# Optimization experiments

Hardware: AMD Instinct MI355X
Metric: run time of the kernel (lower is better)

## Reference

```python
import jax, jax.numpy as jnp
import numpy as np

N = 8192
K = 8192
BS = 128  # quantization block size (elements per codebook)
NE = 8    # codebook entries per block (3-bit indices)


def setup_inputs() -> dict:
    key = jax.random.key(0)
    k1, k2, k3 = jax.random.split(key, 3)
    num_blocks = N * K // BS  # 524288
    n_packed_bytes = num_blocks * BS * 3 // 8  # 25165824
    x = jax.random.normal(k1, (2048, K), dtype=jnp.float32)
    # random packed bytes (values 0..255) -> uniformly random 3-bit indices
    packed_indices = jax.random.randint(k2, (n_packed_bytes,), 0, 256, dtype=jnp.int32)
    codebook = jax.random.normal(k3, (num_blocks, NE), dtype=jnp.float32)
    return {"x": x, "packed_indices": packed_indices, "codebook": codebook}


def _dequantize(packed_indices, codebook):
    num_blocks = codebook.shape[0]
    packed = packed_indices.reshape(-1, 3).astype(jnp.int32)  # (n_groups, 3)
    bits24 = packed[:, 0] | (packed[:, 1] << 8) | (packed[:, 2] << 16)
    shifts = jnp.arange(8, dtype=jnp.int32) * 3
    idx = (bits24[:, None] >> shifts[None, :]) & 7          # (n_groups, 8)
    idx = idx.reshape(num_blocks, BS)                        # (num_blocks, BS)
    # per-block codebook gather: w[b, i] = codebook[b, idx[b, i]]
    w = jnp.take_along_axis(codebook, idx, axis=1)           # (num_blocks, BS)
    return w.reshape(N, K)


def reference(x, packed_indices, codebook):
    w = _dequantize(packed_indices, codebook)  # (N, K) fp32
    y = x @ w.T                                # (batch, N)
    return y
```

## Files before the change

### kernel.cpp

```cpp
#include <hip/hip_runtime.h>
#include <hip/hip_bf16.h>

#define Mdim 2048
#define Ndim 8192
#define Kdim 8192
#define BM 128
#define BN 128
#define BK 64

typedef __bf16 bf16x8 __attribute__((ext_vector_type(8)));
typedef float f32x4 __attribute__((ext_vector_type(4)));
typedef unsigned short ushort8 __attribute__((ext_vector_type(8)));

__device__ __forceinline__ unsigned short f2bf_rne(float f) {
    unsigned u = __float_as_uint(f);
    u += 0x7fffu + ((u >> 16) & 1u);
    return (unsigned short)(u >> 16);
}

#define DQG 1024
__global__ __launch_bounds__(256) void k_dequant(const int* __restrict__ packed,
                                                 const float* __restrict__ cb,
                                                 unsigned short* __restrict__ W) {
    __shared__ int sp[3 * DQG];
    const int t = threadIdx.x;
    const size_t gbase = (size_t)blockIdx.x * DQG;
    const int4* pv = (const int4*)(packed + gbase * 3);
    int4* sv = (int4*)sp;
    sv[t]       = pv[t];
    sv[t + 256] = pv[t + 256];
    sv[t + 512] = pv[t + 512];
    __syncthreads();
#pragma unroll
    for (int c = 0; c < 4; ++c) {
        const int g = t + 256 * c;
        int p0 = sp[3 * g + 0];
        int p1 = sp[3 * g + 1];
        int p2 = sp[3 * g + 2];
        unsigned bits = (unsigned)(p0 & 255) | ((unsigned)(p1 & 255) << 8) |
                        ((unsigned)(p2 & 255) << 16);
        const size_t gg = gbase + g;
        const float4* cv = (const float4*)(cb + ((gg >> 4) << 3));
        float4 c0 = cv[0];
        float4 c1 = cv[1];
        ushort8 o;
#pragma unroll
        for (int i = 0; i < 8; ++i) {
            unsigned id = (bits >> (3 * i)) & 7u;
            float a0 = (id & 1) ? c0.y : c0.x;
            float a1 = (id & 1) ? c0.w : c0.z;
            float a2 = (id & 1) ? c1.y : c1.x;
            float a3 = (id & 1) ? c1.w : c1.z;
            float b0 = (id & 2) ? a1 : a0;
            float b1 = (id & 2) ? a3 : a2;
            float v  = (id & 4) ? b1 : b0;
            o[i] = f2bf_rne(v);
        }
        *(ushort8*)(W + (gg << 3)) = o;
    }
}

__global__ __launch_bounds__(256) void k_cvt(const float* __restrict__ x,
                                             unsigned short* __restrict__ xb) {
    size_t t = (size_t)blockIdx.x * 256 + threadIdx.x;
    const float4* xv = (const float4*)x;
    float4 a = xv[2 * t + 0];
    float4 b = xv[2 * t + 1];
    ushort8 o;
    o[0] = f2bf_rne(a.x); o[1] = f2bf_rne(a.y); o[2] = f2bf_rne(a.z); o[3] = f2bf_rne(a.w);
    o[4] = f2bf_rne(b.x); o[5] = f2bf_rne(b.y); o[6] = f2bf_rne(b.z); o[7] = f2bf_rne(b.w);
    ((ushort8*)xb)[t] = o;
}

__device__ __forceinline__ void gld16(const unsigned short* g, unsigned short* l) {
    __builtin_amdgcn_global_load_lds(
        (const __attribute__((address_space(1))) unsigned int*)g,
        (__attribute__((address_space(3))) unsigned int*)l, 16, 0, 0);
}

__global__ __launch_bounds__(256) void k_gemm(const unsigned short* __restrict__ A,
                                              const unsigned short* __restrict__ B,
                                              float* __restrict__ C) {
    __shared__ unsigned short As[BM * BK];
    __shared__ unsigned short Bs[BN * BK];

    const int tid  = threadIdx.x;
    const int lane = tid & 63;
    const int wave = tid >> 6;
    const int waveM = wave >> 1;
    const int waveN = wave & 1;
    const int bm = blockIdx.y * BM;
    const int bn = blockIdx.x * BN;

    const int srow = tid >> 3;
    const int scol = (((tid & 7) ^ ((tid >> 3) & 7))) * 8;
    const unsigned short* agp = A + (size_t)(bm + srow) * Kdim + scol;
    const unsigned short* bgp = B + (size_t)(bn + srow) * Kdim + scol;
    unsigned short* alp = &As[tid * 8];
    unsigned short* blp = &Bs[tid * 8];

    f32x4 acc[4][4];
    const f32x4 zero = {0.f, 0.f, 0.f, 0.f};
#pragma unroll
    for (int i = 0; i < 4; ++i)
#pragma unroll
        for (int j = 0; j < 4; ++j) acc[i][j] = zero;

    const int r15 = lane & 15;
    const int q   = lane >> 4;
    const int rlo = r15 & 7;

    for (int kt = 0; kt < Kdim; kt += BK) {
#pragma unroll
        for (int j = 0; j < 4; ++j) {
            gld16(agp + (size_t)(j * 32) * Kdim + kt, alp + j * 2048);
            gld16(bgp + (size_t)(j * 32) * Kdim + kt, blp + j * 2048);
        }
        __syncthreads();

#pragma unroll
        for (int kk = 0; kk < 2; ++kk) {
            const int slot = ((kk * 4 + q) ^ rlo) * 8;
            bf16x8 af[4], bfr[4];
#pragma unroll
            for (int i = 0; i < 4; ++i)
                af[i] = *(const bf16x8*)(&As[(waveM * 64 + i * 16 + r15) * BK + slot]);
#pragma unroll
            for (int j = 0; j < 4; ++j)
                bfr[j] = *(const bf16x8*)(&Bs[(waveN * 64 + j * 16 + r15) * BK + slot]);
#pragma unroll
            for (int i = 0; i < 4; ++i)
#pragma unroll
                for (int j = 0; j < 4; ++j)
                    acc[i][j] = __builtin_amdgcn_mfma_f32_16x16x32_bf16(
                        af[i], bfr[j], acc[i][j], 0, 0, 0);
        }
        __syncthreads();
    }

#pragma unroll
    for (int i = 0; i < 4; ++i) {
#pragma unroll
        for (int j = 0; j < 4; ++j) {
            int row = bm + waveM * 64 + i * 16 + q * 4;
            int col = bn + waveN * 64 + j * 16 + r15;
            float* outp = C + (size_t)row * Ndim + col;
#pragma unroll
            for (int r = 0; r < 4; ++r)
                outp[(size_t)r * Ndim] = acc[i][j][r];
        }
    }
}

extern "C" void kernel_launch(void* const* d_in, const int* in_sizes, int n_in,
                              void* d_out, int out_size, void* d_ws, size_t ws_size,
                              hipStream_t stream) {
    const float* x      = (const float*)d_in[0];
    const int*   packed = (const int*)d_in[1];
    const float* cb     = (const float*)d_in[2];
    float* out = (float*)d_out;

    unsigned short* Wb = (unsigned short*)d_ws;
    unsigned short* Xb = (unsigned short*)d_ws + (size_t)Ndim * Kdim;

    k_dequant<<<8192, 256, 0, stream>>>(packed, cb, Wb);
    k_cvt<<<8192, 256, 0, stream>>>(x, Xb);
    dim3 grid(Ndim / BN, Mdim / BM);
    k_gemm<<<grid, 256, 0, stream>>>(Xb, Wb, out);
}
```

Measured before the change: 529.0 us.

## Switch GEMM to 32x32x16 MFMA with new LDS swizzle and fuse prep kernels

Replaces the 16x16x32 bf16 MFMA tiling with 32x32x16 MFMA (2x2 accumulators of 16 floats per wave), which needs fewer LDS fragment reads per FLOP. It adds an XOR swizzle matched to the 32-row fragment reads to avoid LDS bank conflicts. It also merges the dequantization and x-to-bf16 conversion kernels into one launch, with each extra block converting four chunks of x. The cost is a new output store pattern and more complex indexing.

```diff
diff --git a/kernel.cpp b/kernel.cpp
--- a/kernel.cpp
+++ b/kernel.cpp
@@ -9,7 +9,7 @@
 #define BK 64
 
 typedef __bf16 bf16x8 __attribute__((ext_vector_type(8)));
-typedef float f32x4 __attribute__((ext_vector_type(4)));
+typedef float f32x16 __attribute__((ext_vector_type(16)));
 typedef unsigned short ushort8 __attribute__((ext_vector_type(8)));
 
 __device__ __forceinline__ unsigned short f2bf_rne(float f) {
@@ -19,57 +19,64 @@
 }
 
 #define DQG 1024
-__global__ __launch_bounds__(256) void k_dequant(const int* __restrict__ packed,
-                                                 const float* __restrict__ cb,
-                                                 unsigned short* __restrict__ W) {
+__global__ __launch_bounds__(256) void k_prep(const int* __restrict__ packed,
+                                              const float* __restrict__ cb,
+                                              const float* __restrict__ x,
+                                              unsigned short* __restrict__ W,
+                                              unsigned short* __restrict__ xb) {
     __shared__ int sp[3 * DQG];
     const int t = threadIdx.x;
-    const size_t gbase = (size_t)blockIdx.x * DQG;
-    const int4* pv = (const int4*)(packed + gbase * 3);
-    int4* sv = (int4*)sp;
-    sv[t]       = pv[t];
-    sv[t + 256] = pv[t + 256];
-    sv[t + 512] = pv[t + 512];
-    __syncthreads();
+    if (blockIdx.x < 8192) {
+        const size_t gbase = (size_t)blockIdx.x * DQG;
+        const int4* pv = (const int4*)(packed + gbase * 3);
+        int4* sv = (int4*)sp;
+        sv[t]       = pv[t];
+        sv[t + 256] = pv[t + 256];
+        sv[t + 512] = pv[t + 512];
+        __syncthreads();
 #pragma unroll
-    for (int c = 0; c < 4; ++c) {
-        const int g = t + 256 * c;
-        int p0 = sp[3 * g + 0];
-        int p1 = sp[3 * g + 1];
-        int p2 = sp[3 * g + 2];
-        unsigned bits = (unsigned)(p0 & 255) | ((unsigned)(p1 & 255) << 8) |
-                        ((unsigned)(p2 & 255) << 16);
-        const size_t gg = gbase + g;
-        const float4* cv = (const float4*)(cb + ((gg >> 4) << 3));
-        float4 c0 = cv[0];
-        float4 c1 = cv[1];
-        ushort8 o;
+        for (int c = 0; c < 4; ++c) {
+            const int g = t + 256 * c;
+            int p0 = sp[3 * g + 0];
+            int p1 = sp[3 * g + 1];
+            int p2 = sp[3 * g + 2];
+            unsigned bits = (unsigned)(p0 & 255) | ((unsigned)(p1 & 255) << 8) |
+                            ((unsigned)(p2 & 255) << 16);
+            const size_t gg = gbase + g;
+            const float4* cv = (const float4*)(cb + ((gg >> 4) << 3));
+            float4 c0 = cv[0];
+            float4 c1 = cv[1];
+            ushort8 o;
 #pragma unroll
-        for (int i = 0; i < 8; ++i) {
-            unsigned id = (bits >> (3 * i)) & 7u;
-            float a0 = (id & 1) ? c0.y : c0.x;
-            float a1 = (id & 1) ? c0.w : c0.z;
-            float a2 = (id & 1) ? c1.y : c1.x;
-            float a3 = (id & 1) ? c1.w : c1.z;
-            float b0 = (id & 2) ? a1 : a0;
-            float b1 = (id & 2) ? a3 : a2;
-            float v  = (id & 4) ? b1 : b0;
-            o[i] = f2bf_rne(v);
+            for (int i = 0; i < 8; ++i) {
+                unsigned id = (bits >> (3 * i)) & 7u;
+                float a0 = (id & 1) ? c0.y : c0.x;
+                float a1 = (id & 1) ? c0.w : c0.z;
+                float a2 = (id & 1) ? c1.y : c1.x;
+                float a3 = (id & 1) ? c1.w : c1.z;
+                float b0 = (id & 2) ? a1 : a0;
+                float b1 = (id & 2) ? a3 : a2;
+                float v  = (id & 4) ? b1 : b0;
+                o[i] = f2bf_rne(v);
+            }
+            *(ushort8*)(W + (gg << 3)) = o;
         }
-        *(ushort8*)(W + (gg << 3)) = o;
+    } else {
+        size_t tt = (size_t)(blockIdx.x - 8192) * 256 + t;
+        const float4* xv = (const float4*)x;
+#pragma unroll
+        for (int c = 0; c < 4; ++c) {
+            size_t u = tt + (size_t)524288 * c;
+            float4 a = xv[2 * u + 0];
+            float4 b = xv[2 * u + 1];
+            ushort8 o;
+            o[0] = f2bf_rne(a.x); o[1] = f2bf_rne(a.y);
+            o[2] = f2bf_rne(a.z); o[3] = f2bf_rne(a.w);
+            o[4] = f2bf_rne(b.x); o[5] = f2bf_rne(b.y);
+            o[6] = f2bf_rne(b.z); o[7] = f2bf_rne(b.w);
+            ((ushort8*)xb)[u] = o;
+        }
     }
-}
-
-__global__ __launch_bounds__(256) void k_cvt(const float* __restrict__ x,
-                                             unsigned short* __restrict__ xb) {
-    size_t t = (size_t)blockIdx.x * 256 + threadIdx.x;
-    const float4* xv = (const float4*)x;
-    float4 a = xv[2 * t + 0];
-    float4 b = xv[2 * t + 1];
-    ushort8 o;
-    o[0] = f2bf_rne(a.x); o[1] = f2bf_rne(a.y); o[2] = f2bf_rne(a.z); o[3] = f2bf_rne(a.w);
-    o[4] = f2bf_rne(b.x); o[5] = f2bf_rne(b.y); o[6] = f2bf_rne(b.z); o[7] = f2bf_rne(b.w);
-    ((ushort8*)xb)[t] = o;
 }
 
 __device__ __forceinline__ void gld16(const unsigned short* g, unsigned short* l) {
@@ -77,6 +84,8 @@
         (const __attribute__((address_space(1))) unsigned int*)g,
         (__attribute__((address_space(3))) unsigned int*)l, 16, 0, 0);
 }
+
+__device__ __forceinline__ int fsw(int r) { return (r ^ (r >> 3)) & 7; }
 
 __global__ __launch_bounds__(256) void k_gemm(const unsigned short* __restrict__ A,
                                               const unsigned short* __restrict__ B,
@@ -93,61 +102,75 @@
     const int bn = blockIdx.x * BN;
 
     const int srow = tid >> 3;
-    const int scol = (((tid & 7) ^ ((tid >> 3) & 7))) * 8;
-    const unsigned short* agp = A + (size_t)(bm + srow) * Kdim + scol;
-    const unsigned short* bgp = B + (size_t)(bn + srow) * Kdim + scol;
+    const unsigned short* srcA[4];
+    const unsigned short* srcB[4];
+#pragma unroll
+    for (int j = 0; j < 4; ++j) {
+        int row = j * 32 + srow;
+        int scol = ((tid & 7) ^ fsw(row)) * 8;
+        srcA[j] = A + (size_t)(bm + row) * Kdim + scol;
+        srcB[j] = B + (size_t)(bn + row) * Kdim + scol;
+    }
     unsigned short* alp = &As[tid * 8];
     unsigned short* blp = &Bs[tid * 8];
 
-    f32x4 acc[4][4];
-    const f32x4 zero = {0.f, 0.f, 0.f, 0.f};
+    f32x16 acc[2][2];
 #pragma unroll
-    for (int i = 0; i < 4; ++i)
+    for (int i = 0; i < 2; ++i)
 #pragma unroll
-        for (int j = 0; j < 4; ++j) acc[i][j] = zero;
+        for (int j = 0; j < 2; ++j)
+#pragma unroll
+            for (int r = 0; r < 16; ++r) acc[i][j][r] = 0.f;
 
-    const int r15 = lane & 15;
-    const int q   = lane >> 4;
-    const int rlo = r15 & 7;
+    const int r31 = lane & 31;
+    const int hi  = lane >> 5;
+    int hA[2], hB[2], rowA[2], rowB[2];
+#pragma unroll
+    for (int i = 0; i < 2; ++i) {
+        rowA[i] = waveM * 64 + i * 32 + r31;
+        rowB[i] = waveN * 64 + i * 32 + r31;
+        hA[i] = hi ^ fsw(rowA[i]);
+        hB[i] = hi ^ fsw(rowB[i]);
+    }
 
     for (int kt = 0; kt < Kdim; kt += BK) {
 #pragma unroll
         for (int j = 0; j < 4; ++j) {
-            gld16(agp + (size_t)(j * 32) * Kdim + kt, alp + j * 2048);
-            gld16(bgp + (size_t)(j * 32) * Kdim + kt, blp + j * 2048);
+            gld16(srcA[j] + kt, alp + j * 2048);
+            gld16(srcB[j] + kt, blp + j * 2048);
         }
         __syncthreads();
 
 #pragma unroll
-        for (int kk = 0; kk < 2; ++kk) {
-            const int slot = ((kk * 4 + q) ^ rlo) * 8;
-            bf16x8 af[4], bfr[4];
+        for (int ks = 0; ks < 4; ++ks) {
+            bf16x8 af[2], bfr[2];
 #pragma unroll
-            for (int i = 0; i < 4; ++i)
-                af[i] = *(const bf16x8*)(&As[(waveM * 64 + i * 16 + r15) * BK + slot]);
+            for (int i = 0; i < 2; ++i)
+                af[i] = *(const bf16x8*)(&As[rowA[i] * BK + (((ks << 1) ^ hA[i]) * 8)]);
 #pragma unroll
-            for (int j = 0; j < 4; ++j)
-                bfr[j] = *(const bf16x8*)(&Bs[(waveN * 64 + j * 16 + r15) * BK + slot]);
+            for (int j = 0; j < 2; ++j)
+                bfr[j] = *(const bf16x8*)(&Bs[rowB[j] * BK + (((ks << 1) ^ hB[j]) * 8)]);
 #pragma unroll
-            for (int i = 0; i < 4; ++i)
+            for (int i = 0; i < 2; ++i)
 #pragma unroll
-                for (int j = 0; j < 4; ++j)
-                    acc[i][j] = __builtin_amdgcn_mfma_f32_16x16x32_bf16(
+                for (int j = 0; j < 2; ++j)
+                    acc[i][j] = __builtin_amdgcn_mfma_f32_32x32x16_bf16(
                         af[i], bfr[j], acc[i][j], 0, 0, 0);
         }
         __syncthreads();
     }
 
 #pragma unroll
-    for (int i = 0; i < 4; ++i) {
+    for (int i = 0; i < 2; ++i) {
 #pragma unroll
-        for (int j = 0; j < 4; ++j) {
-            int row = bm + waveM * 64 + i * 16 + q * 4;
-            int col = bn + waveN * 64 + j * 16 + r15;
-            float* outp = C + (size_t)row * Ndim + col;
+        for (int j = 0; j < 2; ++j) {
+            int colg = bn + waveN * 64 + j * 32 + r31;
+            int rowg = bm + waveM * 64 + i * 32 + 4 * hi;
 #pragma unroll
-            for (int r = 0; r < 4; ++r)
-                outp[(size_t)r * Ndim] = acc[i][j][r];
+            for (int r = 0; r < 16; ++r) {
+                int row = rowg + (r & 3) + 8 * (r >> 2);
+                C[(size_t)row * Ndim + colg] = acc[i][j][r];
+            }
         }
     }
 }
@@ -163,8 +186,7 @@
     unsigned short* Wb = (unsigned short*)d_ws;
     unsigned short* Xb = (unsigned short*)d_ws + (size_t)Ndim * Kdim;
 
-    k_dequant<<<8192, 256, 0, stream>>>(packed, cb, Wb);
-    k_cvt<<<8192, 256, 0, stream>>>(x, Xb);
+    k_prep<<<10240, 256, 0, stream>>>(packed, cb, x, Wb, Xb);
     dim3 grid(Ndim / BN, Mdim / BM);
     k_gemm<<<grid, 256, 0, stream>>>(Xb, Wb, out);
 }
```

After: 530.4 us. Within noise of the previous version (+0.3%).
